# Performance work log

Measured on AMD Instinct MI355X. Metric: run time of the kernel, lower is better.

## Reference

```python
import jax, jax.numpy as jnp
import numpy as np

D_MODEL, D_STATE, D_CONV, EXPAND = 1024, 16, 4, 2
D_INNER = EXPAND * D_MODEL            # 2048
DT_RANK = -(-D_MODEL // 16)           # ceil(d_model/16) = 64
B_SZ, L_SEQ = 2, 2048


def setup_inputs() -> dict:
    key = jax.random.key(0)
    ks = jax.random.split(key, 8)
    s = 0.02
    x = jax.random.normal(ks[0], (B_SZ, L_SEQ, D_MODEL), dtype=jnp.float32)
    W_in = jax.random.normal(ks[1], (D_MODEL, 2 * D_INNER), dtype=jnp.float32) * s
    conv_w = jax.random.normal(ks[2], (D_INNER, 1, D_CONV), dtype=jnp.float32) * 0.1  # depthwise (O,I/g,K)
    conv_b = jnp.zeros((D_INNER,), dtype=jnp.float32)
    W_x = jax.random.normal(ks[3], (D_INNER, DT_RANK + 2 * D_STATE), dtype=jnp.float32) * s
    W_dt = jax.random.normal(ks[4], (DT_RANK, D_INNER), dtype=jnp.float32) * s
    b_dt = jax.random.normal(ks[5], (D_INNER,), dtype=jnp.float32) * 0.1
    A_log = jnp.log(jnp.tile(jnp.arange(1, D_STATE + 1, dtype=jnp.float32), (D_INNER, 1)))  # (d_in, n)
    D_param = jnp.ones((D_INNER,), dtype=jnp.float32)
    W_out = jax.random.normal(ks[6], (D_INNER, D_MODEL), dtype=jnp.float32) * s
    return {"x": x, "W_in": W_in, "conv_w": conv_w, "conv_b": conv_b,
            "W_x": W_x, "W_dt": W_dt, "b_dt": b_dt, "A_log": A_log,
            "D_param": D_param, "W_out": W_out}


def _mamba(x, W_in, conv_w, conv_b, W_x, W_dt, b_dt, A_log, D_param, W_out):
    b, l, _ = x.shape
    d_in, n = A_log.shape
    dt_rank = W_dt.shape[0]
    d_conv = conv_w.shape[-1]

    xr = x @ W_in                                  # (b, l, 2*d_in)
    xs, res = xr[..., :d_in], xr[..., d_in:]

    # causal depthwise conv1d (left pad d_conv-1, truncate to l)
    xc = jnp.transpose(xs, (0, 2, 1))              # (b, d_in, l)
    xc = jax.lax.conv_general_dilated(
        xc, conv_w, window_strides=(1,), padding=[(d_conv - 1, 0)],
        dimension_numbers=("NCH", "OIH", "NCH"), feature_group_count=d_in)
    xc = xc + conv_b[None, :, None]
    xc = jnp.transpose(xc, (0, 2, 1))              # (b, l, d_in)
    xc = jax.nn.silu(xc)

    # SSM parameterization
    x_dbl = xc @ W_x                               # (b, l, dt_rank + 2n)
    delta = jax.nn.softplus(x_dbl[..., :dt_rank] @ W_dt + b_dt)   # (b, l, d_in)
    Bm = x_dbl[..., dt_rank:dt_rank + n]           # (b, l, n)
    Cm = x_dbl[..., dt_rank + n:]                  # (b, l, n)
    A = -jnp.exp(A_log)                            # (d_in, n)

    deltaA = jnp.exp(jnp.einsum("bld,dn->bldn", delta, A))        # (b, l, d_in, n)
    dBu = jnp.einsum("bld,bld,bln->bldn", delta, xc, Bm)          # (b, l, d_in, n)

    def step(h, inp):
        dA_t, dBu_t, C_t = inp                     # (b,d,n), (b,d,n), (b,n)
        h = dA_t * h + dBu_t
        y_t = jnp.einsum("bdn,bn->bd", h, C_t)
        return h, y_t

    h0 = jnp.zeros((b, d_in, n), dtype=xc.dtype)
    _, ys = jax.lax.scan(
        step, h0,
        (jnp.transpose(deltaA, (1, 0, 2, 3)),
         jnp.transpose(dBu, (1, 0, 2, 3)),
         jnp.transpose(Cm, (1, 0, 2))))
    y = jnp.transpose(ys, (1, 0, 2)) + xc * D_param  # (b, l, d_in)

    y = y * jax.nn.silu(res)
    return y @ W_out                               # (b, l, d_model)


def reference(x, W_in, conv_w, conv_b, W_x, W_dt, b_dt, A_log, D_param, W_out):
    return _mamba(x, W_in, conv_w, conv_b, W_x, W_dt, b_dt, A_log, D_param, W_out)
```

## Files before the change

kernel.cpp:

```cpp
#include <hip/hip_runtime.h>
#include <math.h>

#define B_SZ    2
#define L_SEQ   2048
#define D_MODEL 1024
#define D_INNER 2048
#define D_STATE 16
#define DT_RANK 64
#define MM      (B_SZ * L_SEQ)
#define NCH     64
#define CLEN    (L_SEQ / NCH)
#define PFD     8

typedef _Float16 h8v __attribute__((ext_vector_type(8)));
typedef _Float16 h4v __attribute__((ext_vector_type(4)));
typedef float f32x4 __attribute__((ext_vector_type(4)));

__device__ __forceinline__ void gload16(const void* g, void* l) {
    __builtin_amdgcn_global_load_lds((const __attribute__((address_space(1))) void*)g,
                                     (__attribute__((address_space(3))) void*)l, 16, 0, 0);
}

__global__ __launch_bounds__(256) void prep(const float* __restrict__ x,
                                            _Float16* __restrict__ xf16,
                                            const float* __restrict__ W_in,
                                            _Float16* __restrict__ WinT,
                                            const float* __restrict__ W_x,
                                            _Float16* __restrict__ WxT,
                                            const float* __restrict__ W_dt,
                                            _Float16* __restrict__ WdtT,
                                            const float* __restrict__ W_out,
                                            _Float16* __restrict__ WoutT,
                                            const float* __restrict__ cw,
                                            float* __restrict__ cwT) {
    __shared__ float t[32][33];
    const int b = blockIdx.x;
    const float* W; _Float16* T; int K, N, tile;
    if (b < 4096)      { W = W_in;  T = WinT;  K = 1024; N = 4096; tile = b; }
    else if (b < 4288) { W = W_x;   T = WxT;   K = 2048; N = 96;   tile = b - 4096; }
    else if (b < 4416) { W = W_dt;  T = WdtT;  K = 64;   N = 2048; tile = b - 4288; }
    else if (b < 6464) { W = W_out; T = WoutT; K = 2048; N = 1024; tile = b - 4416; }
    else if (b < 10560) {
        int idx = (b - 6464) * 256 + threadIdx.x;
        float4 v = ((const float4*)x)[idx];
        h4v h = {(_Float16)v.x, (_Float16)v.y, (_Float16)v.z, (_Float16)v.w};
        *(h4v*)(xf16 + (size_t)idx * 4) = h;
        return;
    } else {
        for (int i = threadIdx.x; i < D_INNER * 4; i += 256) {
            int d = i >> 2, k = i & 3;
            cwT[k * D_INNER + d] = cw[i];
        }
        return;
    }
    const int ntx = N / 32;
    const int k0 = (tile / ntx) * 32, n0 = (tile % ntx) * 32;
    #pragma unroll
    for (int i = 0; i < 4; ++i) {
        int idx = threadIdx.x + i * 256;
        int r = idx >> 5, c = idx & 31;
        t[r][c] = W[(size_t)(k0 + r) * N + n0 + c];
    }
    __syncthreads();
    #pragma unroll
    for (int i = 0; i < 4; ++i) {
        int idx = threadIdx.x + i * 256;
        int n = idx >> 5, k = idx & 31;
        T[(size_t)(n0 + n) * K + k0 + k] = (_Float16)t[k][n];
    }
}

#define MF(d, a, b) d = __builtin_amdgcn_mfma_f32_16x16x32_f16(a, b, d, 0, 0, 0)
#define PH16(mb, A0, A1, A2, A3) \
    MF(acc[(mb)+0][0], A0, bF0); MF(acc[(mb)+0][1], A0, bF1); \
    MF(acc[(mb)+0][2], A0, bF2); MF(acc[(mb)+0][3], A0, bF3); \
    MF(acc[(mb)+1][0], A1, bF0); MF(acc[(mb)+1][1], A1, bF1); \
    MF(acc[(mb)+1][2], A1, bF2); MF(acc[(mb)+1][3], A1, bF3); \
    MF(acc[(mb)+2][0], A2, bF0); MF(acc[(mb)+2][1], A2, bF1); \
    MF(acc[(mb)+2][2], A2, bF2); MF(acc[(mb)+2][3], A2, bF3); \
    MF(acc[(mb)+3][0], A3, bF0); MF(acc[(mb)+3][1], A3, bF1); \
    MF(acc[(mb)+3][2], A3, bF2); MF(acc[(mb)+3][3], A3, bF3);

__global__ __launch_bounds__(512, 2) void gemm_k1(const _Float16* __restrict__ A,
                                                  const _Float16* __restrict__ Bt,
                                                  _Float16* __restrict__ H,
                                                  _Float16* __restrict__ Hg) {
    __shared__ _Float16 smem[65536];
    char* smb = (char*)smem;

    const int tid  = threadIdx.x;
    const int wave = tid >> 6, lane = tid & 63;
    const int wm = wave >> 2, wn = wave & 3;
    const int lm = lane & 15, lq = lane >> 4;
    const int bm = blockIdx.y * 256, bn = blockIdx.x * 256;

    const int psl = (lq ^ ((lm >> 1) & 3)) << 4;
    const int rA0 = ((wm * 128 + lm) << 6) + psl;
    const int rB0 = 16384 + ((wn * 64 + lm) << 6) + psl;

    const int srow  = lane >> 2;
    const int sslot = (lane & 3) ^ ((lane >> 3) & 3);
    const _Float16* pA = A  + (size_t)(bm + wave * 16 + srow) * 1024 + sslot * 8;
    const _Float16* pB = Bt + (size_t)(bn + wave * 16 + srow) * 1024 + sslot * 8;
    const int wq = wave * 1024;

    f32x4 acc[8][4];
    #pragma unroll
    for (int i = 0; i < 8; ++i)
        #pragma unroll
        for (int j = 0; j < 4; ++j) acc[i][j] = (f32x4){0.f, 0.f, 0.f, 0.f};

    #pragma unroll
    for (int s = 0; s < 3; ++s) {
        const int bo = s << 15;
        const size_t ko = (size_t)s * 32;
        gload16(pA + ko,          smb + bo + wq);
        gload16(pA + ko + 131072, smb + bo + 8192 + wq);
        gload16(pB + ko,          smb + bo + 16384 + wq);
        gload16(pB + ko + 131072, smb + bo + 24576 + wq);
    }
    asm volatile("s_waitcnt vmcnt(8)" ::: "memory");
    __builtin_amdgcn_s_barrier();

    for (int t = 0; t < 32; ++t) {
        const char* buf = smb + ((t & 3) << 15);
        h8v aF0, aF1, aF2, aF3, bF0, bF1, bF2, bF3;

        aF0 = *(const h8v*)(buf + rA0);
        aF1 = *(const h8v*)(buf + rA0 + 1024);
        aF2 = *(const h8v*)(buf + rA0 + 2048);
        aF3 = *(const h8v*)(buf + rA0 + 3072);
        bF0 = *(const h8v*)(buf + rB0);
        bF1 = *(const h8v*)(buf + rB0 + 1024);
        bF2 = *(const h8v*)(buf + rB0 + 2048);
        bF3 = *(const h8v*)(buf + rB0 + 3072);
        if (t <= 28) {
            const int nb = ((t + 3) & 3) << 15;
            const size_t kn = (size_t)(t + 3) * 32;
            gload16(pA + kn,          smb + nb + wq);
            gload16(pA + kn + 131072, smb + nb + 8192 + wq);
            gload16(pB + kn,          smb + nb + 16384 + wq);
            gload16(pB + kn + 131072, smb + nb + 24576 + wq);
        }
        __builtin_amdgcn_s_barrier();
        asm volatile("s_waitcnt lgkmcnt(0)" ::: "memory");
        __builtin_amdgcn_s_setprio(1);
        PH16(0, aF0, aF1, aF2, aF3);
        __builtin_amdgcn_s_setprio(0);
        __builtin_amdgcn_s_barrier();

        aF0 = *(const h8v*)(buf + rA0 + 4096);
        aF1 = *(const h8v*)(buf + rA0 + 5120);
        aF2 = *(const h8v*)(buf + rA0 + 6144);
        aF3 = *(const h8v*)(buf + rA0 + 7168);
        if (t <= 28)      asm volatile("s_waitcnt vmcnt(8)" ::: "memory");
        else if (t == 29) asm volatile("s_waitcnt vmcnt(4)" ::: "memory");
        else if (t == 30) asm volatile("s_waitcnt vmcnt(0)" ::: "memory");
        __builtin_amdgcn_s_barrier();
        asm volatile("s_waitcnt lgkmcnt(0)" ::: "memory");
        __builtin_amdgcn_s_setprio(1);
        PH16(4, aF0, aF1, aF2, aF3);
        __builtin_amdgcn_s_setprio(0);
        __builtin_amdgcn_s_barrier();
    }

    _Float16* ep = smem + wave * 2048;
    const bool gate = (bn >= 2048);
    _Float16* dst = gate ? Hg : H;
    const int cbase = bn + wn * 64 - (gate ? 2048 : 0);
    #pragma unroll
    for (int mi = 0; mi < 8; ++mi) {
        #pragma unroll
        for (int ni = 0; ni < 4; ++ni)
            #pragma unroll
            for (int r = 0; r < 4; ++r) {
                float v = acc[mi][ni][r];
                if (gate) v = v / (1.f + __expf(-v));
                ep[(lq * 4 + r) * 72 + ni * 16 + lm] = (_Float16)v;
            }
        int rowb = bm + wm * 128 + mi * 16;
        #pragma unroll
        for (int i = 0; i < 2; ++i) {
            int ch = lane + 64 * i;
            int row = ch >> 3, c8 = (ch & 7) * 8;
            *(h8v*)&dst[(size_t)(rowb + row) * 2048 + cbase + c8] =
                *(const h8v*)&ep[row * 72 + c8];
        }
    }
}
#undef MF
#undef PH16

template<int EPI>
__global__ __launch_bounds__(256) void gemm_f16(const _Float16* __restrict__ A,
                                                const _Float16* __restrict__ Bt,
                                                const float* __restrict__ bias,
                                                float* __restrict__ C,
                                                _Float16* __restrict__ H,
                                                _Float16* __restrict__ Hg,
                                                int M, int N, int K, int ldc) {
    __shared__ _Float16 smemh[16384];

    const int tid = threadIdx.x;
    const int wave = tid >> 6, lane = tid & 63;
    const int bm = blockIdx.y * 128, bn = blockIdx.x * 128;

    const int lrow = lane >> 2, pc = lane & 3;
    const int ar = wave * 32 + lrow;
    const size_t gA = (size_t)(bm + ar) * K + ((pc ^ ((ar >> 1) & 3)) * 8);
    const size_t gB = (size_t)(bn + ar) * K + ((pc ^ ((ar >> 1) & 3)) * 8);
    const int lofs = (wave * 32) * 32;

    const int lm = lane & 15, lq = lane >> 4;
    const int rofs = (lq ^ ((lm >> 1) & 3)) * 8;
    const int wm = (wave >> 1) * 64, wn = (wave & 1) * 64;

    f32x4 acc[4][4];
    #pragma unroll
    for (int i = 0; i < 4; ++i)
        #pragma unroll
        for (int j = 0; j < 4; ++j) acc[i][j] = (f32x4){0.f, 0.f, 0.f, 0.f};

    gload16(A + gA, smemh + lofs);
    gload16(A + gA + (size_t)16 * K, smemh + lofs + 16 * 32);
    gload16(Bt + gB, smemh + 8192 + lofs);
    gload16(Bt + gB + (size_t)16 * K, smemh + 8192 + lofs + 16 * 32);
    __syncthreads();

    int kb = 0;
    for (int k0 = 0; k0 < K; k0 += 32, kb ^= 1) {
        if (k0 + 32 < K) {
            int nb = kb ^ 1;
            gload16(A + gA + k0 + 32, smemh + nb * 4096 + lofs);
            gload16(A + gA + k0 + 32 + (size_t)16 * K, smemh + nb * 4096 + lofs + 16 * 32);
            gload16(Bt + gB + k0 + 32, smemh + 8192 + nb * 4096 + lofs);
            gload16(Bt + gB + k0 + 32 + (size_t)16 * K, smemh + 8192 + nb * 4096 + lofs + 16 * 32);
        }

        const _Float16* sA = smemh + kb * 4096;
        const _Float16* sB = smemh + 8192 + kb * 4096;
        h8v fa[4], fb[4];
        #pragma unroll
        for (int i = 0; i < 4; ++i) {
            fa[i] = *(const h8v*)&sA[(wm + i * 16 + lm) * 32 + rofs];
            fb[i] = *(const h8v*)&sB[(wn + i * 16 + lm) * 32 + rofs];
        }
        #pragma unroll
        for (int mi = 0; mi < 4; ++mi)
            #pragma unroll
            for (int ni = 0; ni < 4; ++ni)
                acc[mi][ni] = __builtin_amdgcn_mfma_f32_16x16x32_f16(fa[mi], fb[ni], acc[mi][ni], 0, 0, 0);
        __syncthreads();
    }

    if (EPI == 0) {
        float* ep = (float*)smemh + wave * 1088;
        #pragma unroll
        for (int mi = 0; mi < 4; ++mi) {
            #pragma unroll
            for (int ni = 0; ni < 4; ++ni)
                #pragma unroll
                for (int r = 0; r < 4; ++r)
                    ep[(lq * 4 + r) * 68 + ni * 16 + lm] = acc[mi][ni][r];
            int rowb = bm + wm + mi * 16;
            #pragma unroll
            for (int i = 0; i < 4; ++i) {
                int ch = lane + 64 * i;
                int row = ch >> 4, c4 = (ch & 15) * 4;
                *(float4*)&C[(size_t)(rowb + row) * ldc + bn + wn + c4] =
                    *(const float4*)&ep[row * 68 + c4];
            }
        }
    } else {
        _Float16* ep = smemh + wave * 1152;
        const bool gate = (EPI == 2) && (bn >= 2048);
        _Float16* dst = gate ? Hg : H;
        const int cb = bn + wn - (gate ? 2048 : 0);
        #pragma unroll
        for (int mi = 0; mi < 4; ++mi) {
            #pragma unroll
            for (int ni = 0; ni < 4; ++ni) {
                int col = bn + wn + ni * 16 + lm;
                #pragma unroll
                for (int r = 0; r < 4; ++r) {
                    float v = acc[mi][ni][r];
                    if (EPI == 1) {
                        float a = v + bias[col];
                        v = (a > 20.f) ? a : log1pf(__expf(a));
                    } else if (gate) {
                        v = v / (1.f + __expf(-v));
                    }
                    ep[(lq * 4 + r) * 72 + ni * 16 + lm] = (_Float16)v;
                }
            }
            int rowb = bm + wm + mi * 16;
            #pragma unroll
            for (int i = 0; i < 2; ++i) {
                int ch = lane + 64 * i;
                int row = ch >> 3, c8 = (ch & 7) * 8;
                *(h8v*)&dst[(size_t)(rowb + row) * ldc + cb + c8] =
                    *(const h8v*)&ep[row * 72 + c8];
            }
        }
    }
}

__global__ __launch_bounds__(256) void gemm_xd(const _Float16* __restrict__ xch,
                                               const _Float16* __restrict__ WxT,
                                               _Float16* __restrict__ xdh,
                                               float* __restrict__ Bm,
                                               float* __restrict__ Cm) {
    __shared__ _Float16 sA[64 * 32];
    __shared__ _Float16 sB[96 * 32];
    const int tid = threadIdx.x;
    const int m0 = blockIdx.x * 64;
    const int wave = tid >> 6, lane = tid & 63;
    const int lm = lane & 15, lq = lane >> 4;
    const int rofs = (lq ^ ((lm >> 1) & 3)) * 8;

    const int wr = tid >> 2, wc = tid & 3, c0 = wc * 8;
    const int wofsA = wr * 32 + ((wc ^ ((wr >> 1) & 3)) * 8);
    const int wr2 = 64 + wr;
    const int wofsB2 = wr2 * 32 + ((wc ^ ((wr2 >> 1) & 3)) * 8);

    f32x4 acc[6];
    #pragma unroll
    for (int i = 0; i < 6; ++i) acc[i] = (f32x4){0.f, 0.f, 0.f, 0.f};

    h8v pA = *(const h8v*)(xch + (size_t)(m0 + wr) * D_INNER + c0);
    h8v pB0 = *(const h8v*)(WxT + (size_t)wr * D_INNER + c0);
    h8v pB1 = (tid < 128) ? *(const h8v*)(WxT + (size_t)wr2 * D_INNER + c0) : (h8v)0;

    for (int k0 = 0; k0 < D_INNER; k0 += 32) {
        *(h8v*)&sA[wofsA] = pA;
        *(h8v*)&sB[wofsA] = pB0;
        if (tid < 128) *(h8v*)&sB[wofsB2] = pB1;
        __syncthreads();

        if (k0 + 32 < D_INNER) {
            int kk = k0 + 32 + c0;
            pA = *(const h8v*)(xch + (size_t)(m0 + wr) * D_INNER + kk);
            pB0 = *(const h8v*)(WxT + (size_t)wr * D_INNER + kk);
            if (tid < 128) pB1 = *(const h8v*)(WxT + (size_t)wr2 * D_INNER + kk);
        }

        h8v fa = *(const h8v*)&sA[(wave * 16 + lm) * 32 + rofs];
        #pragma unroll
        for (int nf = 0; nf < 6; ++nf) {
            h8v fb = *(const h8v*)&sB[(nf * 16 + lm) * 32 + rofs];
            acc[nf] = __builtin_amdgcn_mfma_f32_16x16x32_f16(fa, fb, acc[nf], 0, 0, 0);
        }
        __syncthreads();
    }

    #pragma unroll
    for (int nf = 0; nf < 6; ++nf) {
        int col = nf * 16 + lm;
        #pragma unroll
        for (int r = 0; r < 4; ++r) {
            int row = m0 + wave * 16 + lq * 4 + r;
            float v = acc[nf][r];
            if (col < 64)      xdh[(size_t)row * 64 + col] = (_Float16)v;
            else if (col < 80) Bm[(size_t)row * 16 + (col - 64)] = v;
            else               Cm[(size_t)row * 16 + (col - 80)] = v;
        }
    }
}

__global__ __launch_bounds__(256) void conv_silu(const _Float16* __restrict__ xsh,
                                                 const float* __restrict__ cwT,
                                                 const float* __restrict__ cb,
                                                 _Float16* __restrict__ xch) {
    int idx = blockIdx.x * 256 + threadIdx.x;
    int d0 = (idx * 8) & (D_INNER - 1);
    int m  = (idx * 8) >> 11;
    int l  = m & (L_SEQ - 1);
    float acc[8];
    {
        float4 c0 = *(const float4*)&cb[d0];
        float4 c1 = *(const float4*)&cb[d0 + 4];
        acc[0] = c0.x; acc[1] = c0.y; acc[2] = c0.z; acc[3] = c0.w;
        acc[4] = c1.x; acc[5] = c1.y; acc[6] = c1.z; acc[7] = c1.w;
    }
    #pragma unroll
    for (int k = 0; k < 4; ++k) {
        int ll = l - 3 + k;
        if (ll >= 0) {
            h8v v = *(const h8v*)(xsh + (size_t)(m - 3 + k) * D_INNER + d0);
            float4 w0 = *(const float4*)&cwT[k * D_INNER + d0];
            float4 w1 = *(const float4*)&cwT[k * D_INNER + d0 + 4];
            acc[0] += (float)v[0] * w0.x; acc[1] += (float)v[1] * w0.y;
            acc[2] += (float)v[2] * w0.z; acc[3] += (float)v[3] * w0.w;
            acc[4] += (float)v[4] * w1.x; acc[5] += (float)v[5] * w1.y;
            acc[6] += (float)v[6] * w1.z; acc[7] += (float)v[7] * w1.w;
        }
    }
    h8v o;
    #pragma unroll
    for (int j = 0; j < 8; ++j) {
        float s = acc[j] / (1.f + __expf(-acc[j]));
        o[j] = (_Float16)s;
    }
    *(h8v*)(xch + (size_t)idx * 8) = o;
}

__global__ __launch_bounds__(256) void scan_part1(const _Float16* __restrict__ deltah,
                                                  const _Float16* __restrict__ xch,
                                                  const float* __restrict__ Bm,
                                                  const float* __restrict__ A_log,
                                                  float* __restrict__ hlocal,
                                                  float* __restrict__ Ssum) {
    const int t = threadIdx.x;
    const int d = blockIdx.x * 256 + t;
    const int c = blockIdx.y;
    const int b = blockIdx.z;

    float An[16];
    {
        const float4* ap = (const float4*)(A_log + (size_t)d * 16);
        #pragma unroll
        for (int q = 0; q < 4; ++q) {
            float4 v = ap[q];
            An[q * 4 + 0] = -__expf(v.x); An[q * 4 + 1] = -__expf(v.y);
            An[q * 4 + 2] = -__expf(v.z); An[q * 4 + 3] = -__expf(v.w);
        }
    }
    const float An0 = An[0];
    bool fast = An0 < 0.f;
    #pragma unroll
    for (int n = 0; n < 16; ++n)
        fast = fast && (fabsf(An[n] - (float)(n + 1) * An0) < 1e-3f * fabsf(An[n]));

    __shared__ float sB[CLEN][16];
    {
        size_t l0 = (size_t)(b * L_SEQ + c * CLEN) * 16;
        #pragma unroll
        for (int i = 0; i < (CLEN * 16) / 256; ++i) {
            int idx = t + i * 256;
            sB[idx >> 4][idx & 15] = Bm[l0 + idx];
        }
    }
    __syncthreads();

    float h[16];
    #pragma unroll
    for (int n = 0; n < 16; ++n) h[n] = 0.f;
    float S = 0.f;

    size_t base = (size_t)(b * L_SEQ + c * CLEN) * D_INNER + d;
    float bd[PFD], bx[PFD];
    #pragma unroll
    for (int i = 0; i < PFD; ++i) {
        bd[i] = (float)deltah[base + (size_t)i * D_INNER];
        bx[i] = (float)xch[base + (size_t)i * D_INNER];
    }

    if (fast) {
        for (int jb = 0; jb < CLEN; jb += PFD) {
            #pragma unroll
            for (int i = 0; i < PFD; ++i) {
                int j = jb + i;
                float dv = bd[i], xv = bx[i];
                int jn = j + PFD;
                if (jn < CLEN) {
                    bd[i] = (float)deltah[base + (size_t)jn * D_INNER];
                    bx[i] = (float)xch[base + (size_t)jn * D_INNER];
                }
                S += dv;
                float dbx = dv * xv;
                float r = __expf(dv * An0);
                float pw = r;
                #pragma unroll
                for (int n = 0; n < 16; ++n) {
                    h[n] = pw * h[n] + dbx * sB[j][n];
                    pw *= r;
                }
            }
        }
    } else {
        for (int jb = 0; jb < CLEN; jb += PFD) {
            #pragma unroll
            for (int i = 0; i < PFD; ++i) {
                int j = jb + i;
                float dv = bd[i], xv = bx[i];
                int jn = j + PFD;
                if (jn < CLEN) {
                    bd[i] = (float)deltah[base + (size_t)jn * D_INNER];
                    bx[i] = (float)xch[base + (size_t)jn * D_INNER];
                }
                S += dv;
                float dbx = dv * xv;
                #pragma unroll
                for (int n = 0; n < 16; ++n)
                    h[n] = __expf(dv * An[n]) * h[n] + dbx * sB[j][n];
            }
        }
    }

    size_t o = ((size_t)(b * NCH + c) * D_INNER + d) * 16;
    float4* hp = (float4*)(hlocal + o);
    #pragma unroll
    for (int q = 0; q < 4; ++q)
        hp[q] = make_float4(h[q * 4], h[q * 4 + 1], h[q * 4 + 2], h[q * 4 + 3]);
    Ssum[(size_t)(b * NCH + c) * D_INNER + d] = S;
}

__global__ __launch_bounds__(256) void scan_combine(const float* __restrict__ hlocal,
                                                    const float* __restrict__ Ssum,
                                                    const float* __restrict__ A_log,
                                                    float* __restrict__ h0buf) {
    int gid = blockIdx.x * 256 + threadIdx.x;
    int n = gid & 15;
    int d = (gid >> 4) & (D_INNER - 1);
    int b = gid >> 15;
    float An = -__expf(A_log[(size_t)d * 16 + n]);
    float H = 0.f;
    float pS[4], pH[4];
    #pragma unroll
    for (int i = 0; i < 4; ++i) {
        size_t sc = (size_t)(b * NCH + i) * D_INNER + d;
        pS[i] = Ssum[sc];
        pH[i] = hlocal[sc * 16 + n];
    }
    for (int cb = 0; cb < NCH; cb += 4) {
        #pragma unroll
        for (int i = 0; i < 4; ++i) {
            int c = cb + i;
            float S = pS[i], hl = pH[i];
            int cn = c + 4;
            if (cn < NCH) {
                size_t sc = (size_t)(b * NCH + cn) * D_INNER + d;
                pS[i] = Ssum[sc];
                pH[i] = hlocal[sc * 16 + n];
            }
            size_t o = ((size_t)(b * NCH + c) * D_INNER + d) * 16 + n;
            h0buf[o] = H;
            H = __expf(An * S) * H + hl;
        }
    }
}

__global__ __launch_bounds__(256) void scan_part2(const _Float16* __restrict__ deltah,
                                                  const _Float16* __restrict__ xch,
                                                  const float* __restrict__ Bm,
                                                  const float* __restrict__ Cm,
                                                  const float* __restrict__ h0buf,
                                                  const float* __restrict__ A_log,
                                                  const float* __restrict__ Dp,
                                                  const _Float16* __restrict__ sresh,
                                                  _Float16* __restrict__ yhalf) {
    const int t = threadIdx.x;
    const int d = blockIdx.x * 256 + t;
    const int c = blockIdx.y;
    const int b = blockIdx.z;

    float An[16];
    {
        const float4* ap = (const float4*)(A_log + (size_t)d * 16);
        #pragma unroll
        for (int q = 0; q < 4; ++q) {
            float4 v = ap[q];
            An[q * 4 + 0] = -__expf(v.x); An[q * 4 + 1] = -__expf(v.y);
            An[q * 4 + 2] = -__expf(v.z); An[q * 4 + 3] = -__expf(v.w);
        }
    }
    const float An0 = An[0];
    bool fast = An0 < 0.f;
    #pragma unroll
    for (int n = 0; n < 16; ++n)
        fast = fast && (fabsf(An[n] - (float)(n + 1) * An0) < 1e-3f * fabsf(An[n]));

    __shared__ float sB[CLEN][16];
    __shared__ float sC[CLEN][16];
    {
        size_t l0 = (size_t)(b * L_SEQ + c * CLEN) * 16;
        #pragma unroll
        for (int i = 0; i < (CLEN * 16) / 256; ++i) {
            int idx = t + i * 256;
            sB[idx >> 4][idx & 15] = Bm[l0 + idx];
            sC[idx >> 4][idx & 15] = Cm[l0 + idx];
        }
    }
    __syncthreads();

    float h[16];
    {
        size_t o = ((size_t)(b * NCH + c) * D_INNER + d) * 16;
        const float4* hp = (const float4*)(h0buf + o);
        #pragma unroll
        for (int q = 0; q < 4; ++q) {
            float4 v = hp[q];
            h[q * 4 + 0] = v.x; h[q * 4 + 1] = v.y;
            h[q * 4 + 2] = v.z; h[q * 4 + 3] = v.w;
        }
    }
    const float Dv = Dp[d];

    size_t base = (size_t)(b * L_SEQ + c * CLEN) * D_INNER + d;
    float bd[PFD], bx[PFD], bg[PFD];
    #pragma unroll
    for (int i = 0; i < PFD; ++i) {
        bd[i] = (float)deltah[base + (size_t)i * D_INNER];
        bx[i] = (float)xch[base + (size_t)i * D_INNER];
        bg[i] = (float)sresh[base + (size_t)i * D_INNER];
    }

    if (fast) {
        for (int jb = 0; jb < CLEN; jb += PFD) {
            #pragma unroll
            for (int i = 0; i < PFD; ++i) {
                int j = jb + i;
                float dv = bd[i], xv = bx[i], gv = bg[i];
                int jn = j + PFD;
                if (jn < CLEN) {
                    bd[i] = (float)deltah[base + (size_t)jn * D_INNER];
                    bx[i] = (float)xch[base + (size_t)jn * D_INNER];
                    bg[i] = (float)sresh[base + (size_t)jn * D_INNER];
                }
                float dbx = dv * xv;
                float r = __expf(dv * An0);
                float pw = r;
                float y = 0.f;
                #pragma unroll
                for (int n = 0; n < 16; ++n) {
                    h[n] = pw * h[n] + dbx * sB[j][n];
                    y += h[n] * sC[j][n];
                    pw *= r;
                }
                float yv = (y + xv * Dv) * gv;
                yhalf[base + (size_t)j * D_INNER] = (_Float16)yv;
            }
        }
    } else {
        for (int jb = 0; jb < CLEN; jb += PFD) {
            #pragma unroll
            for (int i = 0; i < PFD; ++i) {
                int j = jb + i;
                float dv = bd[i], xv = bx[i], gv = bg[i];
                int jn = j + PFD;
                if (jn < CLEN) {
                    bd[i] = (float)deltah[base + (size_t)jn * D_INNER];
                    bx[i] = (float)xch[base + (size_t)jn * D_INNER];
                    bg[i] = (float)sresh[base + (size_t)jn * D_INNER];
                }
                float dbx = dv * xv;
                float y = 0.f;
                #pragma unroll
                for (int n = 0; n < 16; ++n) {
                    h[n] = __expf(dv * An[n]) * h[n] + dbx * sB[j][n];
                    y += h[n] * sC[j][n];
                }
                float yv = (y + xv * Dv) * gv;
                yhalf[base + (size_t)j * D_INNER] = (_Float16)yv;
            }
        }
    }
}

extern "C" void kernel_launch(void* const* d_in, const int* in_sizes, int n_in,
                              void* d_out, int out_size, void* d_ws, size_t ws_size,
                              hipStream_t stream) {
    const float* x      = (const float*)d_in[0];
    const float* W_in   = (const float*)d_in[1];
    const float* conv_w = (const float*)d_in[2];
    const float* conv_b = (const float*)d_in[3];
    const float* W_x    = (const float*)d_in[4];
    const float* W_dt   = (const float*)d_in[5];
    const float* b_dt   = (const float*)d_in[6];
    const float* A_log  = (const float*)d_in[7];
    const float* D_par  = (const float*)d_in[8];
    const float* W_out  = (const float*)d_in[9];
    float* out = (float*)d_out;

    char* wsb = (char*)d_ws;
    _Float16*  xsh    = (_Float16*)(wsb + 0);
    _Float16*  sresh  = (_Float16*)(wsb + 16777216);
    _Float16*  deltah = (_Float16*)(wsb + 33554432);
    _Float16*  xch    = (_Float16*)(wsb + 50331648);
    _Float16*  xf16   = (_Float16*)(wsb + 67108864);
    _Float16*  WinT   = (_Float16*)(wsb + 75497472);
    _Float16*  yhalf  = (_Float16*)(wsb + 67108864);
    _Float16*  WxT    = (_Float16*)(wsb + 83886080);
    _Float16*  WdtT   = (_Float16*)(wsb + 84279296);
    _Float16*  xdh    = (_Float16*)(wsb + 84541440);
    float*     Bbuf   = (float*)(wsb + 85065728);
    float*     Cbuf   = (float*)(wsb + 85327872);
    float*     Ssum   = (float*)(wsb + 85590016);
    float*     hloc   = (float*)(wsb + 86638592);
    float*     h0buf  = (float*)(wsb + 103415808);
    _Float16*  WoutT  = (_Float16*)(wsb + 120193024);
    float*     cwT    = (float*)(wsb + 124387328);

    dim3 blk(256);

    prep<<<dim3(10561), blk, 0, stream>>>(x, xf16, W_in, WinT, W_x, WxT,
                                          W_dt, WdtT, W_out, WoutT, conv_w, cwT);
    gemm_k1<<<dim3(16, 16), dim3(512), 0, stream>>>(xf16, WinT, xsh, sresh);
    conv_silu<<<dim3((size_t)MM * D_INNER / 8 / 256), blk, 0, stream>>>(xsh, cwT, conv_b, xch);
    gemm_xd<<<dim3(MM / 64), blk, 0, stream>>>(xch, WxT, xdh, Bbuf, Cbuf);
    gemm_f16<1><<<dim3(16, 32), blk, 0, stream>>>(
        xdh, WdtT, b_dt, nullptr, deltah, nullptr, MM, D_INNER, DT_RANK, D_INNER);
    scan_part1<<<dim3(D_INNER / 256, NCH, B_SZ), blk, 0, stream>>>(deltah, xch, Bbuf, A_log, hloc, Ssum);
    scan_combine<<<dim3(B_SZ * D_INNER * 16 / 256), blk, 0, stream>>>(hloc, Ssum, A_log, h0buf);
    scan_part2<<<dim3(D_INNER / 256, NCH, B_SZ), blk, 0, stream>>>(deltah, xch, Bbuf, Cbuf, h0buf, A_log, D_par, sresh, yhalf);
    gemm_f16<0><<<dim3(8, 32), blk, 0, stream>>>(
        yhalf, WoutT, nullptr, out, nullptr, nullptr, MM, D_MODEL, D_INNER, D_MODEL);
}
```

Measured before the change: 322.7 us.

## Software-pipeline LDS fragment loads across k-steps in the in-projection GEMM

Restructures the main loop of the in-projection GEMM so that the A and B fragments for the next k-step are read from LDS while the second half of the current step's MFMAs runs, using double-buffered B registers and a loop unrolled by two. Explicit lgkmcnt waits and one barrier per half-step are removed, and the compiler is left to order waits. The aim is to hide LDS read latency behind matrix instructions and cut barrier stalls. In exchange it uses more VGPRs, which at 512 threads with two blocks per CU could cause spills, and the relaxed synchronisation adds risk of LDS read-after-write hazards.

```diff
diff --git a/kernel.cpp b/kernel.cpp
--- a/kernel.cpp
+++ b/kernel.cpp
@@ -71,15 +71,61 @@
 }
 
 #define MF(d, a, b) d = __builtin_amdgcn_mfma_f32_16x16x32_f16(a, b, d, 0, 0, 0)
-#define PH16(mb, A0, A1, A2, A3) \
-    MF(acc[(mb)+0][0], A0, bF0); MF(acc[(mb)+0][1], A0, bF1); \
-    MF(acc[(mb)+0][2], A0, bF2); MF(acc[(mb)+0][3], A0, bF3); \
-    MF(acc[(mb)+1][0], A1, bF0); MF(acc[(mb)+1][1], A1, bF1); \
-    MF(acc[(mb)+1][2], A1, bF2); MF(acc[(mb)+1][3], A1, bF3); \
-    MF(acc[(mb)+2][0], A2, bF0); MF(acc[(mb)+2][1], A2, bF1); \
-    MF(acc[(mb)+2][2], A2, bF2); MF(acc[(mb)+2][3], A2, bF3); \
-    MF(acc[(mb)+3][0], A3, bF0); MF(acc[(mb)+3][1], A3, bF1); \
-    MF(acc[(mb)+3][2], A3, bF2); MF(acc[(mb)+3][3], A3, bF3);
+
+#define KSTEP(t, CUR, NXT)                                                          \
+{                                                                                   \
+    const char* buf = smb + (((t) & 3) << 15);                                      \
+                                                             \
+    __builtin_amdgcn_s_barrier();                                                   \
+    a47[0] = *(const h8v*)(buf + rA0 + 4096);                                       \
+    a47[1] = *(const h8v*)(buf + rA0 + 5120);                                       \
+    a47[2] = *(const h8v*)(buf + rA0 + 6144);                                       \
+    a47[3] = *(const h8v*)(buf + rA0 + 7168);                                       \
+    if ((t) <= 28) {                                                                \
+        const int nb = (((t) + 3) & 3) << 15;                                       \
+        const size_t kn = (size_t)((t) + 3) * 32;                                   \
+        gload16(pA + kn,          smb + nb + wq);                                   \
+        gload16(pA + kn + 131072, smb + nb + 8192 + wq);                            \
+        gload16(pB + kn,          smb + nb + 16384 + wq);                           \
+        gload16(pB + kn + 131072, smb + nb + 24576 + wq);                           \
+    }                                                                               \
+    __builtin_amdgcn_s_setprio(1);                                                  \
+    MF(acc[0][0], a03[0], b4[CUR][0]); MF(acc[0][1], a03[0], b4[CUR][1]);           \
+    MF(acc[0][2], a03[0], b4[CUR][2]); MF(acc[0][3], a03[0], b4[CUR][3]);           \
+    MF(acc[1][0], a03[1], b4[CUR][0]); MF(acc[1][1], a03[1], b4[CUR][1]);           \
+    MF(acc[1][2], a03[1], b4[CUR][2]); MF(acc[1][3], a03[1], b4[CUR][3]);           \
+    MF(acc[2][0], a03[2], b4[CUR][0]); MF(acc[2][1], a03[2], b4[CUR][1]);           \
+    MF(acc[2][2], a03[2], b4[CUR][2]); MF(acc[2][3], a03[2], b4[CUR][3]);           \
+    MF(acc[3][0], a03[3], b4[CUR][0]); MF(acc[3][1], a03[3], b4[CUR][1]);           \
+    MF(acc[3][2], a03[3], b4[CUR][2]); MF(acc[3][3], a03[3], b4[CUR][3]);           \
+    __builtin_amdgcn_s_setprio(0);                                                  \
+                                                             \
+    if ((t) <= 28)      asm volatile("s_waitcnt vmcnt(8)" ::: "memory");            \
+    else if ((t) == 29) asm volatile("s_waitcnt vmcnt(4)" ::: "memory");            \
+    else if ((t) == 30) asm volatile("s_waitcnt vmcnt(0)" ::: "memory");            \
+    __builtin_amdgcn_s_barrier();                                                   \
+    if ((t) < 31) {                                                                 \
+        const char* nbuf = smb + ((((t) + 1) & 3) << 15);                           \
+        a03[0] = *(const h8v*)(nbuf + rA0);                                         \
+        a03[1] = *(const h8v*)(nbuf + rA0 + 1024);                                  \
+        a03[2] = *(const h8v*)(nbuf + rA0 + 2048);                                  \
+        a03[3] = *(const h8v*)(nbuf + rA0 + 3072);                                  \
+        b4[NXT][0] = *(const h8v*)(nbuf + rB0);                                     \
+        b4[NXT][1] = *(const h8v*)(nbuf + rB0 + 1024);                              \
+        b4[NXT][2] = *(const h8v*)(nbuf + rB0 + 2048);                              \
+        b4[NXT][3] = *(const h8v*)(nbuf + rB0 + 3072);                              \
+    }                                                                               \
+    __builtin_amdgcn_s_setprio(1);                                                  \
+    MF(acc[4][0], a47[0], b4[CUR][0]); MF(acc[4][1], a47[0], b4[CUR][1]);           \
+    MF(acc[4][2], a47[0], b4[CUR][2]); MF(acc[4][3], a47[0], b4[CUR][3]);           \
+    MF(acc[5][0], a47[1], b4[CUR][0]); MF(acc[5][1], a47[1], b4[CUR][1]);           \
+    MF(acc[5][2], a47[1], b4[CUR][2]); MF(acc[5][3], a47[1], b4[CUR][3]);           \
+    MF(acc[6][0], a47[2], b4[CUR][0]); MF(acc[6][1], a47[2], b4[CUR][1]);           \
+    MF(acc[6][2], a47[2], b4[CUR][2]); MF(acc[6][3], a47[2], b4[CUR][3]);           \
+    MF(acc[7][0], a47[3], b4[CUR][0]); MF(acc[7][1], a47[3], b4[CUR][1]);           \
+    MF(acc[7][2], a47[3], b4[CUR][2]); MF(acc[7][3], a47[3], b4[CUR][3]);           \
+    __builtin_amdgcn_s_setprio(0);                                                  \
+}
 
 __global__ __launch_bounds__(512, 2) void gemm_k1(const _Float16* __restrict__ A,
                                                   const _Float16* __restrict__ Bt,
@@ -109,6 +155,8 @@
     for (int i = 0; i < 8; ++i)
         #pragma unroll
         for (int j = 0; j < 4; ++j) acc[i][j] = (f32x4){0.f, 0.f, 0.f, 0.f};
+
+    h8v a03[4], a47[4], b4[2][4];
 
     #pragma unroll
     for (int s = 0; s < 3; ++s) {
@@ -121,47 +169,18 @@
     }
     asm volatile("s_waitcnt vmcnt(8)" ::: "memory");
     __builtin_amdgcn_s_barrier();
-
-    for (int t = 0; t < 32; ++t) {
-        const char* buf = smb + ((t & 3) << 15);
-        h8v aF0, aF1, aF2, aF3, bF0, bF1, bF2, bF3;
-
-        aF0 = *(const h8v*)(buf + rA0);
-        aF1 = *(const h8v*)(buf + rA0 + 1024);
-        aF2 = *(const h8v*)(buf + rA0 + 2048);
-        aF3 = *(const h8v*)(buf + rA0 + 3072);
-        bF0 = *(const h8v*)(buf + rB0);
-        bF1 = *(const h8v*)(buf + rB0 + 1024);
-        bF2 = *(const h8v*)(buf + rB0 + 2048);
-        bF3 = *(const h8v*)(buf + rB0 + 3072);
-        if (t <= 28) {
-            const int nb = ((t + 3) & 3) << 15;
-            const size_t kn = (size_t)(t + 3) * 32;
-            gload16(pA + kn,          smb + nb + wq);
-            gload16(pA + kn + 131072, smb + nb + 8192 + wq);
-            gload16(pB + kn,          smb + nb + 16384 + wq);
-            gload16(pB + kn + 131072, smb + nb + 24576 + wq);
-        }
-        __builtin_amdgcn_s_barrier();
-        asm volatile("s_waitcnt lgkmcnt(0)" ::: "memory");
-        __builtin_amdgcn_s_setprio(1);
-        PH16(0, aF0, aF1, aF2, aF3);
-        __builtin_amdgcn_s_setprio(0);
-        __builtin_amdgcn_s_barrier();
-
-        aF0 = *(const h8v*)(buf + rA0 + 4096);
-        aF1 = *(const h8v*)(buf + rA0 + 5120);
-        aF2 = *(const h8v*)(buf + rA0 + 6144);
-        aF3 = *(const h8v*)(buf + rA0 + 7168);
-        if (t <= 28)      asm volatile("s_waitcnt vmcnt(8)" ::: "memory");
-        else if (t == 29) asm volatile("s_waitcnt vmcnt(4)" ::: "memory");
-        else if (t == 30) asm volatile("s_waitcnt vmcnt(0)" ::: "memory");
-        __builtin_amdgcn_s_barrier();
-        asm volatile("s_waitcnt lgkmcnt(0)" ::: "memory");
-        __builtin_amdgcn_s_setprio(1);
-        PH16(4, aF0, aF1, aF2, aF3);
-        __builtin_amdgcn_s_setprio(0);
-        __builtin_amdgcn_s_barrier();
+    a03[0] = *(const h8v*)(smb + rA0);
+    a03[1] = *(const h8v*)(smb + rA0 + 1024);
+    a03[2] = *(const h8v*)(smb + rA0 + 2048);
+    a03[3] = *(const h8v*)(smb + rA0 + 3072);
+    b4[0][0] = *(const h8v*)(smb + rB0);
+    b4[0][1] = *(const h8v*)(smb + rB0 + 1024);
+    b4[0][2] = *(const h8v*)(smb + rB0 + 2048);
+    b4[0][3] = *(const h8v*)(smb + rB0 + 3072);
+
+    for (int tt = 0; tt < 32; tt += 2) {
+        KSTEP(tt,     0, 1);
+        KSTEP(tt + 1, 1, 0);
     }
 
     _Float16* ep = smem + wave * 2048;
@@ -189,7 +208,7 @@
     }
 }
 #undef MF
-#undef PH16
+#undef KSTEP
 
 template<int EPI>
 __global__ __launch_bounds__(256) void gemm_f16(const _Float16* __restrict__ A,
```

Measured after the change: 319.5 us. No clear change (-1.0%).
